# Optimization experiments

Measured on AMD Instinct MI355X. Metric: run time of the kernel, lower is better.

The kernel has to match this reference:

```python
import jax, jax.numpy as jnp
import numpy as np

B, T = 4, 512
IN, OUT, D, HID = 80, 4096, 512, 1024
E, NB, LPB = 4, 2, 4
NL = NB * LPB
H, M = 8, 64
LB, LA, SL, SR = 4, 1, 2, 1


def setup_inputs():
    key = jax.random.key(0)
    it = iter(jax.random.split(key, 40))
    def nrm(shape, s=0.02):
        return jax.random.normal(next(it), shape, jnp.float32) * s
    return {
        'x': jax.random.normal(next(it), (B, T, IN), jnp.float32),
        'seq_len': jax.random.randint(next(it), (B,), T // 2, T + 1),
        'emb_w1': nrm((IN, HID)), 'emb_b1': jnp.zeros((HID,), jnp.float32),
        'emb_w2': nrm((HID, D)), 'emb_wo': nrm((D, OUT)),
        'f0_w1': nrm((E, IN, HID)), 'f0_b1': jnp.zeros((E, HID), jnp.float32),
        'f0_w2': nrm((E, HID, D)), 'f0_router': nrm((D, E)),
        'f0_fb': nrm((LB, D), 0.1), 'f0_fa': nrm((LA, D), 0.1),
        'f_w1': nrm((NL - 1, E, D, HID)), 'f_b1': jnp.zeros((NL - 1, E, HID), jnp.float32),
        'f_w2': nrm((NL - 1, E, HID, D)), 'f_router': nrm((NL - 1, D, E)),
        'f_fb': nrm((NL - 1, LB, D), 0.1), 'f_fa': nrm((NL - 1, LA, D), 0.1),
        'attn_wq': nrm((NB, D, D)), 'attn_wk': nrm((NB, D, D)),
        'attn_wv': nrm((NB, D, D)), 'attn_wo': nrm((NB, D, D)),
        'attn_mk': nrm((NB, M, D)), 'attn_mv': nrm((NB, M, D)),
        'ln_g': jnp.ones((NB, D), jnp.float32), 'ln_b': jnp.zeros((NB, D), jnp.float32),
        'out_w': nrm((D, OUT)), 'out_b': jnp.zeros((OUT,), jnp.float32),
    }


def _fsmn_memory(p, fb, fa):
    # m[t] = p[t] + sum_k fb[k]*p[t-(k+1)*SL] + sum_j fa[j]*p[t+(j+1)*SR]  (depthwise)
    m = p
    for k in range(fb.shape[0]):
        off = (k + 1) * SL
        past = jnp.pad(p, ((0, 0), (off, 0), (0, 0)))[:, :p.shape[1]]
        m = m + past * fb[k]
    for j in range(fa.shape[0]):
        off = (j + 1) * SR
        fut = jnp.pad(p, ((0, 0), (0, off), (0, 0)))[:, off:]
        m = m + fut * fa[j]
    return m


def _pe(dtype):
    pos = jnp.arange(T, dtype=jnp.float32)[:, None]
    div = jnp.exp(jnp.arange(0, D, 2, dtype=jnp.float32) * (-np.log(10000.0) / D))
    pe = jnp.zeros((T, D), jnp.float32)
    pe = pe.at[:, 0::2].set(jnp.sin(pos * div)).at[:, 1::2].set(jnp.cos(pos * div))
    return pe.astype(dtype)


def _layernorm(x, g, b):
    mu = jnp.mean(x, -1, keepdims=True)
    var = jnp.var(x, -1, keepdims=True)
    return (x - mu) * jax.lax.rsqrt(var + 1e-5) * g + b


def reference(x, seq_len, emb_w1, emb_b1, emb_w2, emb_wo,
              f0_w1, f0_b1, f0_w2, f0_router, f0_fb, f0_fa,
              f_w1, f_b1, f_w2, f_router, f_fb, f_fa,
              attn_wq, attn_wk, attn_wv, attn_wo, attn_mk, attn_mv,
              ln_g, ln_b, out_w, out_b):
    tok_mask = jnp.arange(T)[None, :] < seq_len[:, None]  # [B,T] valid frames

    # embed sub-network (router features; detached as in Net.forward)
    embed = jax.nn.relu(x @ emb_w1 + emb_b1) @ emb_w2      # [B,T,D]
    embed_out = embed @ emb_wo                             # [B,T,OUT]
    embed_r = jax.lax.stop_gradient(embed)

    def moe_fsmn(xi, w1, b1, w2, router, fb, fa, skip):
        gates = jax.nn.softmax(embed_r @ router, axis=-1)  # [B,T,E]
        g = jnp.max(gates, axis=-1)
        disp = jax.nn.one_hot(jnp.argmax(gates, -1), E, dtype=xi.dtype) * g[..., None]
        h = jax.nn.relu(jnp.einsum('bti,eih->beth', xi, w1) + b1[None, :, None, :])
        p = jnp.einsum('beth,ehd->betd', h, w2)            # low-rank expert proj
        p = jnp.einsum('bte,betd->btd', disp, p)           # top-1 combine
        m = _fsmn_memory(p, fb, fa)
        if skip:
            m = m + xi
        imp = jnp.sum(gates * tok_mask[..., None].astype(gates.dtype), axis=(0, 1))
        aux = jnp.var(imp) / (jnp.mean(imp) ** 2 + 1e-9)   # importance cv^2
        return m, aux

    def attention(xi, wq, wk, wv, wo, mk, mv, g, b):
        dh = D // H
        q = (xi @ wq).reshape(B, T, H, dh)
        k = jnp.concatenate([xi @ wk, jnp.broadcast_to(mk, (B, M, D))], 1).reshape(B, T + M, H, dh)
        v = jnp.concatenate([xi @ wv, jnp.broadcast_to(mv, (B, M, D))], 1).reshape(B, T + M, H, dh)
        scores = jnp.einsum('bthd,bshd->bhts', q, k) / np.sqrt(dh).astype(np.float32)
        key_ok = jnp.concatenate([tok_mask, jnp.ones((B, M), bool)], 1)  # memory keys never masked
        scores = jnp.where(key_ok[:, None, None, :], scores, jnp.float32(-1e9))
        a = jax.nn.softmax(scores, -1)
        o = jnp.einsum('bhts,bshd->bthd', a, v).reshape(B, T, D) @ wo
        return _layernorm(xi + o, g, b)

    auxes = []
    cur = x
    li = 0
    for blk in range(NB):
        for _ in range(LPB):
            if li == 0:
                cur, aux = moe_fsmn(cur, f0_w1, f0_b1, f0_w2, f0_router, f0_fb, f0_fa, False)
            else:
                j = li - 1
                cur, aux = moe_fsmn(cur, f_w1[j], f_b1[j], f_w2[j], f_router[j], f_fb[j], f_fa[j], True)
            auxes.append(aux)
            li += 1
        if blk == 0:
            cur = cur + _pe(cur.dtype)[None]
        cur = attention(cur, attn_wq[blk], attn_wk[blk], attn_wv[blk], attn_wo[blk],
                        attn_mk[blk], attn_mv[blk], ln_g[blk], ln_b[blk])
    out = cur @ out_w + out_b
    return out, embed_out, jnp.stack(auxes).sum()
```

## Files before the change

kernel.cpp:

```cpp
#include <hip/hip_runtime.h>
#include <hip/hip_bf16.h>


typedef __bf16 bf16x8 __attribute__((ext_vector_type(8)));
typedef float f32x4 __attribute__((ext_vector_type(4)));

#define B_ 4
#define T_ 512
#define IN_ 80
#define OUT_ 4096
#define D_ 512
#define HID_ 1024
#define E_ 4
#define H_ 8
#define DH_ 64
#define M_ 64
#define BT_ (B_ * T_)
#define TKV_ (T_ + M_)
#define RBLK_ (BT_ / 4)

__device__ __forceinline__ unsigned pk2(float a, float b) {
    unsigned short ua = __builtin_bit_cast(unsigned short, (__bf16)a);
    unsigned short ub = __builtin_bit_cast(unsigned short, (__bf16)b);
    return (unsigned)ua | ((unsigned)ub << 16);
}
__device__ __forceinline__ unsigned pkh2(__bf16 a, __bf16 b) {
    unsigned short ua = __builtin_bit_cast(unsigned short, a);
    unsigned short ub = __builtin_bit_cast(unsigned short, b);
    return (unsigned)ua | ((unsigned)ub << 16);
}

__global__ __launch_bounds__(256) void gemm80_k(
    const float* __restrict__ A,
    const float* __restrict__ Bw,
    const float* __restrict__ bias,
    float* __restrict__ C)
{
    __shared__ float As[80][68];
    __shared__ float Bs[80][68];
    int m0 = blockIdx.y * 64, n0 = blockIdx.x * 64;
    int tid = threadIdx.x;
#pragma unroll
    for (int i = 0; i < 5; i++) {
        int idx = tid + 256 * i;
        int m = idx / 20, c = idx % 20;
        float4 f = *(const float4*)&A[(size_t)(m0 + m) * 80 + c * 4];
        As[c * 4 + 0][m] = f.x; As[c * 4 + 1][m] = f.y;
        As[c * 4 + 2][m] = f.z; As[c * 4 + 3][m] = f.w;
    }
#pragma unroll
    for (int i = 0; i < 5; i++) {
        int idx = tid + 256 * i;
        int k = idx / 16, c = idx % 16;
        float4 f = *(const float4*)&Bw[(size_t)k * 1024 + n0 + c * 4];
        *(float4*)&Bs[k][c * 4] = f;
    }
    __syncthreads();
    int tx = tid & 15, ty = tid >> 4;
    float acc[4][4];
#pragma unroll
    for (int j = 0; j < 4; j++)
#pragma unroll
        for (int i = 0; i < 4; i++) acc[j][i] = 0.f;
#pragma unroll 8
    for (int k = 0; k < 80; k++) {
        float4 a = *(const float4*)&As[k][ty * 4];
        float4 b = *(const float4*)&Bs[k][tx * 4];
        float av[4] = {a.x, a.y, a.z, a.w};
        float bv[4] = {b.x, b.y, b.z, b.w};
#pragma unroll
        for (int j = 0; j < 4; j++)
#pragma unroll
            for (int i = 0; i < 4; i++) acc[j][i] += av[j] * bv[i];
    }
#pragma unroll
    for (int j = 0; j < 4; j++) {
        size_t row = (size_t)(m0 + ty * 4 + j);
        float4 o;
        o.x = fmaxf(acc[j][0] + bias[n0 + tx * 4 + 0], 0.f);
        o.y = fmaxf(acc[j][1] + bias[n0 + tx * 4 + 1], 0.f);
        o.z = fmaxf(acc[j][2] + bias[n0 + tx * 4 + 2], 0.f);
        o.w = fmaxf(acc[j][3] + bias[n0 + tx * 4 + 3], 0.f);
        *(float4*)&C[row * 1024 + n0 + tx * 4] = o;
    }
}

__global__ void wr2_k(const float* __restrict__ w2,
                      const float* __restrict__ r0,
                      const float* __restrict__ rl,
                      float* __restrict__ R2)
{
    int wv = threadIdx.x >> 6, lane = threadIdx.x & 63;
    int h = blockIdx.x * 4 + wv;
    const float* wrow = w2 + (size_t)h * 512;
    float w[8];
#pragma unroll
    for (int i = 0; i < 8; i++) w[i] = wrow[lane + 64 * i];
    for (int l = 0; l < 8; l++) {
        const float* rp = (l == 0) ? r0 : rl + (size_t)(l - 1) * 2048;
        double a0 = 0, a1 = 0, a2 = 0, a3 = 0;
#pragma unroll
        for (int i = 0; i < 8; i++) {
            int d = lane + 64 * i;
            float4 r = *(const float4*)&rp[d * 4];
            a0 += (double)w[i] * (double)r.x;
            a1 += (double)w[i] * (double)r.y;
            a2 += (double)w[i] * (double)r.z;
            a3 += (double)w[i] * (double)r.w;
        }
        for (int off = 32; off; off >>= 1) {
            a0 += __shfl_xor(a0, off); a1 += __shfl_xor(a1, off);
            a2 += __shfl_xor(a2, off); a3 += __shfl_xor(a3, off);
        }
        if (lane == 0) {
            float4 o = make_float4((float)a0, (float)a1, (float)a2, (float)a3);
            *(float4*)&R2[((size_t)l * 1024 + h) * 4] = o;
        }
    }
}

__global__ __launch_bounds__(256) void routerall_k(
    const float* __restrict__ h,
    const float* __restrict__ R2,
    const int* __restrict__ seq_len,
    int* __restrict__ eid,
    float* __restrict__ gatev,
    float* __restrict__ impPart)
{
    __shared__ float impLoc[4][32];
    int wv = threadIdx.x >> 6, lane = threadIdx.x & 63;
    int tok = blockIdx.x * 4 + wv;
    const float* hr = h + (size_t)tok * 1024;
    float acc[8][4];
#pragma unroll
    for (int l = 0; l < 8; l++)
#pragma unroll
        for (int e = 0; e < 4; e++) acc[l][e] = 0.f;
    for (int i = 0; i < 16; i++) {
        int d = lane + 64 * i;
        float hv = hr[d];
#pragma unroll
        for (int l = 0; l < 8; l++) {
            float4 r = *(const float4*)&R2[((size_t)l * 1024 + d) * 4];
            acc[l][0] += hv * r.x; acc[l][1] += hv * r.y;
            acc[l][2] += hv * r.z; acc[l][3] += hv * r.w;
        }
    }
    for (int off = 32; off; off >>= 1) {
#pragma unroll
        for (int l = 0; l < 8; l++)
#pragma unroll
            for (int e = 0; e < 4; e++) acc[l][e] += __shfl_xor(acc[l][e], off);
    }
    if (lane == 0) {
        int b = tok >> 9, t = tok & 511;
        bool valid = t < seq_len[b];
        for (int l = 0; l < 8; l++) {
            float lg[4] = {acc[l][0], acc[l][1], acc[l][2], acc[l][3]};
            float mx = fmaxf(fmaxf(lg[0], lg[1]), fmaxf(lg[2], lg[3]));
            float g[4], s = 0.f;
            for (int e = 0; e < 4; e++) { g[e] = expf(lg[e] - mx); s += g[e]; }
            float inv = 1.f / s;
            int am = 0; float bv = g[0];
            for (int e = 1; e < 4; e++) if (g[e] > bv) { bv = g[e]; am = e; }
            eid[l * BT_ + tok] = am;
            gatev[l * BT_ + tok] = bv * inv;
            for (int e = 0; e < 4; e++)
                impLoc[wv][l * 4 + e] = valid ? g[e] * inv : 0.f;
        }
    }
    __syncthreads();
    int tid = threadIdx.x;
    if (tid < 32) {
        float s = impLoc[0][tid] + impLoc[1][tid] + impLoc[2][tid] + impLoc[3][tid];
        impPart[(size_t)blockIdx.x * 32 + tid] = s;
    }
}

__global__ void cvtw_k(const float* __restrict__ src, __bf16* __restrict__ dst,
                       int nsh, int kpsh, int Ksrc)
{
    int idx = blockIdx.x * 256 + threadIdx.x;
    int cprsh = nsh - 3;
    int row = idx >> cprsh;
    int chunk = idx & ((1 << cprsh) - 1);
    int e = row >> kpsh, k = row & ((1 << kpsh) - 1);
    int n = chunk * 8;
    uint4 pk;
    if (k < Ksrc) {
        const float* sp = src + (((size_t)e * Ksrc + k) << nsh) + n;
        float4 f0 = *(const float4*)sp;
        float4 f1 = *(const float4*)(sp + 4);
        pk = make_uint4(pk2(f0.x, f0.y), pk2(f0.z, f0.w),
                        pk2(f1.x, f1.y), pk2(f1.z, f1.w));
    } else pk = make_uint4(0, 0, 0, 0);
    *(uint4*)&dst[(((size_t)row) << nsh) + n] = pk;
}

__global__ void gathera_k(const float* __restrict__ src, int lda,
                          const int* __restrict__ sorted,
                          __bf16* __restrict__ dst, int kpsh, int Ksrc)
{
    int idx = blockIdx.x * 256 + threadIdx.x;
    int cprsh = kpsh - 3;
    int row = idx >> cprsh;
    int chunk = idx & ((1 << cprsh) - 1);
    int k0 = chunk * 8;
    uint4 pk;
    if (k0 < Ksrc) {
        const float* sp = src + (size_t)sorted[row] * lda + k0;
        float4 f0 = *(const float4*)sp;
        float4 f1 = *(const float4*)(sp + 4);
        pk = make_uint4(pk2(f0.x, f0.y), pk2(f0.z, f0.w),
                        pk2(f1.x, f1.y), pk2(f1.z, f1.w));
    } else pk = make_uint4(0, 0, 0, 0);
    *(uint4*)&dst[((size_t)row << kpsh) + k0] = pk;
}

template<bool W1OUT>
__global__ __launch_bounds__(256) void egemm_k(
    const __bf16* __restrict__ Ag, const __bf16* __restrict__ Bh,
    const float* __restrict__ bias,
    __bf16* __restrict__ Cb, float* __restrict__ Cf,
    int N, int Kpad,
    const int* __restrict__ seg, const int* __restrict__ sorted,
    const float* __restrict__ scale)
{
    __shared__ __align__(16) __bf16 As[2][128 * 64];
    __shared__ __align__(16) __bf16 Bs[2][64 * 64];

    int e = blockIdx.z;
    int row0 = seg[e], cnt = seg[e + 1] - row0;
    int m0 = blockIdx.y * 128;
    if (m0 >= cnt) return;
    int n0 = blockIdx.x * 64;
    const __bf16* Bp = Bh + (size_t)e * Kpad * N;

    int tid = threadIdx.x;
    int arow = tid >> 1, ahalf = tid & 1;
    const __bf16* aptr = Ag + (size_t)(row0 + m0 + arow) * Kpad + ahalf * 32;
    int asb = arow * 64;
    int ac0 = ahalf * 4;
    int arx = arow & 7;
    int bn = tid & 63, bkc = tid >> 6;
    const __bf16* bptr = Bp + n0 + bn;
    int bsb = bn * 64;
    int brx = bn & 7;

    int lane = tid & 63, wid = tid >> 6;
    int wm = wid & 1, wn = wid >> 1;
    int l15 = lane & 15, quad = lane >> 4;

    int aoff[4][2], boff[2][2];
#pragma unroll
    for (int mt = 0; mt < 4; mt++) {
        int m = wm * 64 + mt * 16 + l15;
#pragma unroll
        for (int s = 0; s < 2; s++)
            aoff[mt][s] = m * 64 + (((s * 4 + quad) ^ (m & 7)) * 8);
    }
#pragma unroll
    for (int nt = 0; nt < 2; nt++) {
        int n = wn * 32 + nt * 16 + l15;
#pragma unroll
        for (int s = 0; s < 2; s++)
            boff[nt][s] = n * 64 + (((s * 4 + quad) ^ (n & 7)) * 8);
    }

    f32x4 acc[4][2];
#pragma unroll
    for (int mt = 0; mt < 4; mt++)
#pragma unroll
        for (int nt = 0; nt < 2; nt++)
#pragma unroll
            for (int r = 0; r < 4; r++) acc[mt][nt][r] = 0.f;

    uint4 rA[4]; unsigned rB[8];
    auto stage = [&](int k0) {
#pragma unroll
        for (int j = 0; j < 4; j++) rA[j] = *(const uint4*)(aptr + k0 + j * 8);
#pragma unroll
        for (int c = 0; c < 2; c++) {
            int kk = k0 + (bkc * 2 + c) * 8;
#pragma unroll
            for (int i = 0; i < 4; i++)
                rB[c * 4 + i] = pkh2(bptr[(size_t)(kk + 2 * i) * N],
                                     bptr[(size_t)(kk + 2 * i + 1) * N]);
        }
    };
    auto commit = [&](int buf) {
#pragma unroll
        for (int j = 0; j < 4; j++)
            *(uint4*)&As[buf][asb + (((ac0 + j) ^ arx) * 8)] = rA[j];
#pragma unroll
        for (int c = 0; c < 2; c++)
            *(uint4*)&Bs[buf][bsb + (((bkc * 2 + c) ^ brx) * 8)] =
                make_uint4(rB[c * 4 + 0], rB[c * 4 + 1], rB[c * 4 + 2], rB[c * 4 + 3]);
    };

    stage(0); commit(0); __syncthreads();
    int nt_ = Kpad >> 6;
    for (int t = 0; t < nt_; t++) {
        int buf = t & 1;
        if (t + 1 < nt_) stage((t + 1) << 6);
        bf16x8 af[4][2], bfr[2][2];
#pragma unroll
        for (int mt = 0; mt < 4; mt++)
#pragma unroll
            for (int s = 0; s < 2; s++)
                af[mt][s] = *(const bf16x8*)&As[buf][aoff[mt][s]];
#pragma unroll
        for (int ntx = 0; ntx < 2; ntx++)
#pragma unroll
            for (int s = 0; s < 2; s++)
                bfr[ntx][s] = *(const bf16x8*)&Bs[buf][boff[ntx][s]];
#pragma unroll
        for (int mt = 0; mt < 4; mt++)
#pragma unroll
            for (int ntx = 0; ntx < 2; ntx++)
#pragma unroll
                for (int s = 0; s < 2; s++)
                    acc[mt][ntx] = __builtin_amdgcn_mfma_f32_16x16x32_bf16(
                        af[mt][s], bfr[ntx][s], acc[mt][ntx], 0, 0, 0);
        if (t + 1 < nt_) commit(buf ^ 1);
        __syncthreads();
    }

#pragma unroll
    for (int mt = 0; mt < 4; mt++) {
#pragma unroll
        for (int r = 0; r < 4; r++) {
            int m = m0 + wm * 64 + mt * 16 + quad * 4 + r;
            if (m >= cnt) continue;
            if (W1OUT) {
                size_t ci = (size_t)(row0 + m);
#pragma unroll
                for (int ntx = 0; ntx < 2; ntx++) {
                    int col = n0 + wn * 32 + ntx * 16 + l15;
                    float v = acc[mt][ntx][r] + bias[e * N + col];
                    Cb[ci * N + col] = (__bf16)fmaxf(v, 0.f);
                }
            } else {
                int tok = sorted[row0 + m];
                float sc = scale[tok];
#pragma unroll
                for (int ntx = 0; ntx < 2; ntx++) {
                    int col = n0 + wn * 32 + ntx * 16 + l15;
                    Cf[(size_t)tok * N + col] = acc[mt][ntx][r] * sc;
                }
            }
        }
    }
}

template<bool BIAS>
__global__ __launch_bounds__(256) void dgemm_k(
    const float* __restrict__ A,
    const __bf16* __restrict__ Bh,
    const float* __restrict__ bias,
    float* __restrict__ C,
    int N, int K)
{
    __shared__ __align__(16) __bf16 As[2][128 * 64];
    __shared__ __align__(16) __bf16 Bs[2][64 * 64];

    int m0 = blockIdx.y * 128, n0 = blockIdx.x * 64;
    int tid = threadIdx.x;
    int arow = tid >> 1, ahalf = tid & 1;
    const float* aptr = A + (size_t)(m0 + arow) * K + ahalf * 32;
    int asb = arow * 64, ac0 = ahalf * 4, arx = arow & 7;
    int bn = tid & 63, bkc = tid >> 6;
    const __bf16* bptr = Bh + n0 + bn;
    int bsb = bn * 64, brx = bn & 7;

    int lane = tid & 63, wid = tid >> 6;
    int wm = wid & 1, wn = wid >> 1;
    int l15 = lane & 15, quad = lane >> 4;

    int aoff[4][2], boff[2][2];
#pragma unroll
    for (int mt = 0; mt < 4; mt++) {
        int m = wm * 64 + mt * 16 + l15;
#pragma unroll
        for (int s = 0; s < 2; s++)
            aoff[mt][s] = m * 64 + (((s * 4 + quad) ^ (m & 7)) * 8);
    }
#pragma unroll
    for (int nt = 0; nt < 2; nt++) {
        int n = wn * 32 + nt * 16 + l15;
#pragma unroll
        for (int s = 0; s < 2; s++)
            boff[nt][s] = n * 64 + (((s * 4 + quad) ^ (n & 7)) * 8);
    }

    f32x4 acc[4][2];
#pragma unroll
    for (int mt = 0; mt < 4; mt++)
#pragma unroll
        for (int nt = 0; nt < 2; nt++)
#pragma unroll
            for (int r = 0; r < 4; r++) acc[mt][nt][r] = 0.f;

    uint4 rA[4]; unsigned rB[8];
    auto stage = [&](int k0) {
#pragma unroll
        for (int j = 0; j < 4; j++) {
            float4 f0 = *(const float4*)(aptr + k0 + j * 8);
            float4 f1 = *(const float4*)(aptr + k0 + j * 8 + 4);
            rA[j] = make_uint4(pk2(f0.x, f0.y), pk2(f0.z, f0.w),
                               pk2(f1.x, f1.y), pk2(f1.z, f1.w));
        }
#pragma unroll
        for (int c = 0; c < 2; c++) {
            int kk = k0 + (bkc * 2 + c) * 8;
#pragma unroll
            for (int i = 0; i < 4; i++)
                rB[c * 4 + i] = pkh2(bptr[(size_t)(kk + 2 * i) * N],
                                     bptr[(size_t)(kk + 2 * i + 1) * N]);
        }
    };
    auto commit = [&](int buf) {
#pragma unroll
        for (int j = 0; j < 4; j++)
            *(uint4*)&As[buf][asb + (((ac0 + j) ^ arx) * 8)] = rA[j];
#pragma unroll
        for (int c = 0; c < 2; c++)
            *(uint4*)&Bs[buf][bsb + (((bkc * 2 + c) ^ brx) * 8)] =
                make_uint4(rB[c * 4 + 0], rB[c * 4 + 1], rB[c * 4 + 2], rB[c * 4 + 3]);
    };

    stage(0); commit(0); __syncthreads();
    int nt_ = K >> 6;
    for (int t = 0; t < nt_; t++) {
        int buf = t & 1;
        if (t + 1 < nt_) stage((t + 1) << 6);
        bf16x8 af[4][2], bfr[2][2];
#pragma unroll
        for (int mt = 0; mt < 4; mt++)
#pragma unroll
            for (int s = 0; s < 2; s++)
                af[mt][s] = *(const bf16x8*)&As[buf][aoff[mt][s]];
#pragma unroll
        for (int ntx = 0; ntx < 2; ntx++)
#pragma unroll
            for (int s = 0; s < 2; s++)
                bfr[ntx][s] = *(const bf16x8*)&Bs[buf][boff[ntx][s]];
#pragma unroll
        for (int mt = 0; mt < 4; mt++)
#pragma unroll
            for (int ntx = 0; ntx < 2; ntx++)
#pragma unroll
                for (int s = 0; s < 2; s++)
                    acc[mt][ntx] = __builtin_amdgcn_mfma_f32_16x16x32_bf16(
                        af[mt][s], bfr[ntx][s], acc[mt][ntx], 0, 0, 0);
        if (t + 1 < nt_) commit(buf ^ 1);
        __syncthreads();
    }

#pragma unroll
    for (int mt = 0; mt < 4; mt++) {
#pragma unroll
        for (int r = 0; r < 4; r++) {
            int m = m0 + wm * 64 + mt * 16 + quad * 4 + r;
#pragma unroll
            for (int ntx = 0; ntx < 2; ntx++) {
                int col = n0 + wn * 32 + ntx * 16 + l15;
                float v = acc[mt][ntx][r];
                if (BIAS) v += bias[col];
                C[(size_t)m * N + col] = v;
            }
        }
    }
}

#define MBM 128
#define MBN 64
#define MBK 32
#define LDAS 40

__global__ __launch_bounds__(256) void qkv_k(
    const float* __restrict__ A,
    const __bf16* __restrict__ wq, const __bf16* __restrict__ wk,
    const __bf16* __restrict__ wv,
    float* __restrict__ qo, float* __restrict__ ko, float* __restrict__ vo)
{
    __shared__ __align__(16) __bf16 As[MBM * LDAS];
    __shared__ __align__(16) __bf16 Bs[MBN * LDAS];

    int n0g = blockIdx.x * MBN;
    int which = n0g >> 9;
    int n0 = n0g & 511;
    const __bf16* Bp = (which == 0) ? wq : (which == 1) ? wk : wv;
    float* Cp = (which == 0) ? qo : (which == 1) ? ko : vo;
    int m0 = blockIdx.y * MBM;

    int tid = threadIdx.x;
    int arow = tid >> 1, ahalf = tid & 1;
    const float* aptr = A + (size_t)(m0 + arow) * D_ + ahalf * 16;
    int asw = (arow >> 3) & 3;
    int bn = tid & 63, bkc = tid >> 6;
    int bcs = bkc ^ ((bn >> 3) & 3);

    int lane = tid & 63, wid = tid >> 6;
    int wm = wid & 1, wn = wid >> 1;
    int l15 = lane & 15, quad = lane >> 4;

    int aoff[4], boff[2];
#pragma unroll
    for (int mt = 0; mt < 4; mt++) {
        int m = wm * 64 + mt * 16 + l15;
        aoff[mt] = m * LDAS + (quad ^ ((m >> 3) & 3)) * 8;
    }
#pragma unroll
    for (int nt = 0; nt < 2; nt++) {
        int n = wn * 32 + nt * 16 + l15;
        boff[nt] = n * LDAS + (quad ^ ((n >> 3) & 3)) * 8;
    }

    f32x4 acc[4][2];
#pragma unroll
    for (int mt = 0; mt < 4; mt++)
#pragma unroll
        for (int nt = 0; nt < 2; nt++)
#pragma unroll
            for (int r = 0; r < 4; r++) acc[mt][nt][r] = 0.f;

    for (int k0 = 0; k0 < D_; k0 += MBK) {
#pragma unroll
        for (int cc = 0; cc < 2; cc++) {
            float4 f0 = *(const float4*)(aptr + k0 + cc * 8);
            float4 f1 = *(const float4*)(aptr + k0 + cc * 8 + 4);
            uint4 pk = make_uint4(pk2(f0.x, f0.y), pk2(f0.z, f0.w),
                                  pk2(f1.x, f1.y), pk2(f1.z, f1.w));
            int cs = (ahalf * 2 + cc) ^ asw;
            *(uint4*)&As[arow * LDAS + cs * 8] = pk;
        }
        {
            __bf16 f[8];
            int kk = k0 + bkc * 8;
#pragma unroll
            for (int i = 0; i < 8; i++)
                f[i] = Bp[(size_t)(kk + i) * D_ + n0 + bn];
            uint4 pk = make_uint4(pkh2(f[0], f[1]), pkh2(f[2], f[3]),
                                  pkh2(f[4], f[5]), pkh2(f[6], f[7]));
            *(uint4*)&Bs[bn * LDAS + bcs * 8] = pk;
        }
        __syncthreads();
        bf16x8 af[4], bfm[2];
#pragma unroll
        for (int mt = 0; mt < 4; mt++) af[mt] = *(const bf16x8*)&As[aoff[mt]];
#pragma unroll
        for (int nt = 0; nt < 2; nt++) bfm[nt] = *(const bf16x8*)&Bs[boff[nt]];
#pragma unroll
        for (int mt = 0; mt < 4; mt++)
#pragma unroll
            for (int nt = 0; nt < 2; nt++)
                acc[mt][nt] = __builtin_amdgcn_mfma_f32_16x16x32_bf16(
                    af[mt], bfm[nt], acc[mt][nt], 0, 0, 0);
        __syncthreads();
    }

#pragma unroll
    for (int mt = 0; mt < 4; mt++) {
#pragma unroll
        for (int r = 0; r < 4; r++) {
            int mi = wm * 64 + mt * 16 + quad * 4 + r;
            int m = m0 + mi;
            size_t crow = which ? (size_t)(m + (m >> 9) * M_) : (size_t)m;
#pragma unroll
            for (int nt = 0; nt < 2; nt++) {
                int col = n0 + wn * 32 + nt * 16 + l15;
                Cp[crow * (size_t)D_ + col] = acc[mt][nt][r];
            }
        }
    }
}

__global__ void bucketall_k(const int* __restrict__ eidA, int* __restrict__ sortedA,
                            int* __restrict__ segA)
{
    __shared__ int cnt[E_]; __shared__ int cur[E_];
    int l = blockIdx.x;
    const int* eid = eidA + l * BT_;
    int* sorted = sortedA + l * BT_;
    int* seg = segA + l * 8;
    int tid = threadIdx.x;
    if (tid < E_) cnt[tid] = 0;
    __syncthreads();
    for (int t = tid; t < BT_; t += 256) atomicAdd(&cnt[eid[t]], 1);
    __syncthreads();
    if (tid == 0) {
        int o = 0;
        for (int e = 0; e < E_; e++) { seg[e] = o; cur[e] = o; o += cnt[e]; }
        seg[E_] = o;
    }
    __syncthreads();
    for (int t = tid; t < BT_; t += 256) {
        int pos = atomicAdd(&cur[eid[t]], 1);
        sorted[pos] = t;
    }
}

__global__ void fsmn_k(const float* __restrict__ p, const float* __restrict__ fb,
                       const float* __restrict__ fa, float* __restrict__ cur, int skip)
{
    int idx = blockIdx.x * 256 + threadIdx.x;
    int d = idx & 511;
    int t = (idx >> 9) & 511;
    float m = p[idx];
#pragma unroll
    for (int k = 0; k < 4; k++) {
        int tt = t - 2 * (k + 1);
        if (tt >= 0) m += fb[k * D_ + d] * p[idx - D_ * 2 * (k + 1)];
    }
    if (t + 1 < T_) m += fa[d] * p[idx + D_];
    if (skip) m += cur[idx];
    cur[idx] = m;
}

__global__ void addpe_k(float* __restrict__ cur) {
    int idx = blockIdx.x * 256 + threadIdx.x;
    int d = idx & 511, t = (idx >> 9) & 511;
    float div = expf((float)(d & ~1) * (-9.210340371976184f / (float)D_));
    float ang = (float)t * div;
    cur[idx] += (d & 1) ? cosf(ang) : sinf(ang);
}

__global__ void fillmem_k(const float* __restrict__ mk, const float* __restrict__ mv,
                          float* __restrict__ kbuf, float* __restrict__ vbuf)
{
    int idx = blockIdx.x * 256 + threadIdx.x;
    int d = idx & 511, m = (idx >> 9) & 63, b = idx >> 15;
    size_t row = (size_t)b * TKV_ + T_ + m;
    kbuf[row * D_ + d] = mk[m * D_ + d];
    vbuf[row * D_ + d] = mv[m * D_ + d];
}

#define QR 16
__global__ __launch_bounds__(256) void attn_k(
    const float* __restrict__ q, const float* __restrict__ kbuf,
    const float* __restrict__ vbuf, const int* __restrict__ seq_len,
    float* __restrict__ attno)
{
    __shared__ float kv[64 * 68];
    __shared__ float qs[QR][68];
    __shared__ float sc[QR][584];
    int b = blockIdx.z, h = blockIdx.y, t0 = blockIdx.x * QR;
    int tid = threadIdx.x, w = tid >> 6, lane = tid & 63;
    int r0 = w * 4;
#pragma unroll
    for (int i = 0; i < 4; i++) {
        int idx = tid + 256 * i;
        int r = idx >> 6, d = idx & 63;
        qs[r][d] = q[((size_t)(b * T_) + t0 + r) * D_ + h * DH_ + d] * 0.125f;
    }
    int sl = seq_len[b];
    int ntv = (sl + 63) >> 6;
    int kg = lane & 15, quad = lane >> 4;
    int myrow = r0 + quad;

    for (int ti = 0; ti <= ntv; ti++) {
        int t = (ti < ntv) ? ti : 8;
        int s0 = t * 64;
        __syncthreads();
        {
            const float* kp = kbuf + ((size_t)b * TKV_ + s0 + w * 16) * D_ + h * DH_ + lane;
#pragma unroll
            for (int jj = 0; jj < 4; jj++) {
                float4 kf;
                kf.x = kp[(jj * 4 + 0) * D_];
                kf.y = kp[(jj * 4 + 1) * D_];
                kf.z = kp[(jj * 4 + 2) * D_];
                kf.w = kp[(jj * 4 + 3) * D_];
                *(float4*)&kv[lane * 68 + w * 16 + jj * 4] = kf;
            }
        }
        __syncthreads();
        float a0 = 0, a1 = 0, a2 = 0, a3 = 0;
#pragma unroll 8
        for (int d = 0; d < 64; d++) {
            float4 kf = *(const float4*)&kv[d * 68 + kg * 4];
            float qv = qs[myrow][d];
            a0 = fmaf(qv, kf.x, a0);
            a1 = fmaf(qv, kf.y, a1);
            a2 = fmaf(qv, kf.z, a2);
            a3 = fmaf(qv, kf.w, a3);
        }
        int sb = s0 + kg * 4;
        float4 o;
        o.x = (sb + 0 >= T_ || sb + 0 < sl) ? a0 : -1e9f;
        o.y = (sb + 1 >= T_ || sb + 1 < sl) ? a1 : -1e9f;
        o.z = (sb + 2 >= T_ || sb + 2 < sl) ? a2 : -1e9f;
        o.w = (sb + 3 >= T_ || sb + 3 < sl) ? a3 : -1e9f;
        *(float4*)&sc[myrow][s0 + kg * 4] = o;
    }
    __syncthreads();

    float inv[4];
#pragma unroll
    for (int r = 0; r < 4; r++) {
        float mx = -1e30f;
        for (int ti = 0; ti <= ntv; ti++) {
            int s0 = ((ti < ntv) ? ti : 8) * 64;
            mx = fmaxf(mx, sc[r0 + r][s0 + lane]);
        }
        for (int off = 32; off; off >>= 1) mx = fmaxf(mx, __shfl_xor(mx, off));
        float sum = 0.f;
        for (int ti = 0; ti <= ntv; ti++) {
            int s0 = ((ti < ntv) ? ti : 8) * 64;
            float e2 = expf(sc[r0 + r][s0 + lane] - mx);
            sc[r0 + r][s0 + lane] = e2; sum += e2;
        }
        for (int off = 32; off; off >>= 1) sum += __shfl_xor(sum, off);
        inv[r] = 1.f / sum;
    }

    float o0 = 0, o1 = 0, o2 = 0, o3 = 0;
    for (int ti = 0; ti <= ntv; ti++) {
        int t = (ti < ntv) ? ti : 8;
        int s0 = t * 64;
        __syncthreads();
#pragma unroll
        for (int i = 0; i < 16; i++) {
            int idx = tid + 256 * i;
            int key = idx >> 6, d = idx & 63;
            kv[key * 68 + d] = vbuf[((size_t)b * TKV_ + s0 + key) * D_ + h * DH_ + d];
        }
        __syncthreads();
#pragma unroll 4
        for (int g = 0; g < 16; g++) {
            float4 p0 = *(const float4*)&sc[r0 + 0][s0 + g * 4];
            float4 p1 = *(const float4*)&sc[r0 + 1][s0 + g * 4];
            float4 p2 = *(const float4*)&sc[r0 + 2][s0 + g * 4];
            float4 p3 = *(const float4*)&sc[r0 + 3][s0 + g * 4];
            float v0 = kv[(g * 4 + 0) * 68 + lane];
            float v1 = kv[(g * 4 + 1) * 68 + lane];
            float v2 = kv[(g * 4 + 2) * 68 + lane];
            float v3 = kv[(g * 4 + 3) * 68 + lane];
            o0 += p0.x * v0 + p0.y * v1 + p0.z * v2 + p0.w * v3;
            o1 += p1.x * v0 + p1.y * v1 + p1.z * v2 + p1.w * v3;
            o2 += p2.x * v0 + p2.y * v1 + p2.z * v2 + p2.w * v3;
            o3 += p3.x * v0 + p3.y * v1 + p3.z * v2 + p3.w * v3;
        }
    }
    size_t base = ((size_t)(b * T_) + t0 + r0) * D_ + h * DH_ + lane;
    attno[base + 0 * D_] = o0 * inv[0];
    attno[base + 1 * D_] = o1 * inv[1];
    attno[base + 2 * D_] = o2 * inv[2];
    attno[base + 3 * D_] = o3 * inv[3];
}

__global__ void ln_k(const float* __restrict__ o, const float* __restrict__ g,
                     const float* __restrict__ bb, float* __restrict__ cur)
{
    int w = threadIdx.x >> 6, lane = threadIdx.x & 63;
    size_t row = (size_t)(blockIdx.x * 4 + w);
    float v[8]; float s = 0.f;
#pragma unroll
    for (int i = 0; i < 8; i++) {
        int d = lane + 64 * i;
        v[i] = cur[row * D_ + d] + o[row * D_ + d];
        s += v[i];
    }
    for (int off = 32; off; off >>= 1) s += __shfl_xor(s, off);
    float mu = s * (1.f / D_);
    float vs = 0.f;
#pragma unroll
    for (int i = 0; i < 8; i++) { float dd = v[i] - mu; vs += dd * dd; }
    for (int off = 32; off; off >>= 1) vs += __shfl_xor(vs, off);
    float rstd = rsqrtf(vs * (1.f / D_) + 1e-5f);
#pragma unroll
    for (int i = 0; i < 8; i++) {
        int d = lane + 64 * i;
        cur[row * D_ + d] = (v[i] - mu) * rstd * g[d] + bb[d];
    }
}

__global__ __launch_bounds__(256) void aux_k(const float* __restrict__ impPart,
                                             float* __restrict__ outp)
{
    __shared__ float red[8][32];
    __shared__ float imp[32];
    int tid = threadIdx.x;
    int c = tid & 31, p = tid >> 5;
    float s = 0.f;
    for (int b = p; b < RBLK_; b += 8) s += impPart[(size_t)b * 32 + c];
    red[p][c] = s;
    __syncthreads();
    if (tid < 32) {
        float t = 0.f;
#pragma unroll
        for (int i = 0; i < 8; i++) t += red[i][tid];
        imp[tid] = t;
    }
    __syncthreads();
    if (tid == 0) {
        float total = 0.f;
        for (int l = 0; l < 8; l++) {
            const float* ip = imp + l * 4;
            float m = (ip[0] + ip[1] + ip[2] + ip[3]) * 0.25f;
            float var = 0.f;
            for (int e = 0; e < 4; e++) { float d = ip[e] - m; var += d * d; }
            var *= 0.25f;
            total += var / (m * m + 1e-9f);
        }
        *outp = total;
    }
}

extern "C" void kernel_launch(void* const* d_in, const int* in_sizes, int n_in,
                              void* d_out, int out_size, void* d_ws, size_t ws_size,
                              hipStream_t stream)
{
    (void)in_sizes; (void)n_in; (void)out_size; (void)ws_size;
    const float* x        = (const float*)d_in[0];
    const int*   seqlen   = (const int*)d_in[1];
    const float* emb_w1   = (const float*)d_in[2];
    const float* emb_b1   = (const float*)d_in[3];
    const float* emb_w2   = (const float*)d_in[4];
    const float* emb_wo   = (const float*)d_in[5];
    const float* f0_w1    = (const float*)d_in[6];
    const float* f0_b1    = (const float*)d_in[7];
    const float* f0_w2    = (const float*)d_in[8];
    const float* f0_router= (const float*)d_in[9];
    const float* f0_fb    = (const float*)d_in[10];
    const float* f0_fa    = (const float*)d_in[11];
    const float* f_w1     = (const float*)d_in[12];
    const float* f_b1     = (const float*)d_in[13];
    const float* f_w2     = (const float*)d_in[14];
    const float* f_router = (const float*)d_in[15];
    const float* f_fb     = (const float*)d_in[16];
    const float* f_fa     = (const float*)d_in[17];
    const float* attn_wq  = (const float*)d_in[18];
    const float* attn_wk  = (const float*)d_in[19];
    const float* attn_wv  = (const float*)d_in[20];
    const float* attn_wo  = (const float*)d_in[21];
    const float* attn_mk  = (const float*)d_in[22];
    const float* attn_mv  = (const float*)d_in[23];
    const float* ln_g     = (const float*)d_in[24];
    const float* ln_b     = (const float*)d_in[25];
    const float* out_w    = (const float*)d_in[26];
    const float* out_b    = (const float*)d_in[27];

    float* out0 = (float*)d_out;
    float* out1 = out0 + (size_t)BT_ * OUT_;
    float* out2 = out1 + (size_t)BT_ * OUT_;

    float* fws = (float*)d_ws;
    size_t o = 0;
    float* embedF = fws + o; o += (size_t)BT_ * D_;
    float* curB   = fws + o; o += (size_t)BT_ * D_;
    float* hbuf   = fws + o; o += (size_t)BT_ * HID_;
    float* pbuf   = fws + o; o += (size_t)BT_ * D_;
    float* kbuf   = fws + o; o += (size_t)B_ * TKV_ * D_;
    float* vbuf   = fws + o; o += (size_t)B_ * TKV_ * D_;
    float* gatev  = fws + o; o += (size_t)8 * BT_;
    float* impPart= fws + o; o += (size_t)RBLK_ * 32;
    float* R2     = fws + o; o += (size_t)8 * 1024 * 4;
    int* eid     = (int*)(fws + o); o += (size_t)8 * BT_;
    int* sortedA = (int*)(fws + o); o += (size_t)8 * BT_;
    int* segA    = (int*)(fws + o); o += 64;
    __bf16* Ag    = (__bf16*)hbuf;
    __bf16* hbufh = (__bf16*)(hbuf + (size_t)BT_ * D_ / 2);
    __bf16* w1h   = (__bf16*)kbuf;
    __bf16* w2h   = (__bf16*)vbuf;
    __bf16* w2e_h = (__bf16*)vbuf;
    __bf16* woe_h = (__bf16*)kbuf;
    __bf16* outw_h= (__bf16*)kbuf;
    __bf16* wqh   = (__bf16*)embedF;
    __bf16* wkh   = wqh + (size_t)D_ * D_;
    __bf16* wvh   = wkh + (size_t)D_ * D_;
    __bf16* woh   = wvh + (size_t)D_ * D_;
    float* qbuf  = pbuf;
    float* attno = hbuf;
    float* tmpo  = hbuf + (size_t)BT_ * D_;

    gemm80_k<<<dim3(HID_ / 64, BT_ / 64, 1), 256, 0, stream>>>(x, emb_w1, emb_b1, hbuf);
    wr2_k<<<256, 256, 0, stream>>>(emb_w2, f0_router, f_router, R2);
    routerall_k<<<RBLK_, 256, 0, stream>>>(hbuf, R2, seqlen, eid, gatev, impPart);
    bucketall_k<<<8, 256, 0, stream>>>(eid, sortedA, segA);
    cvtw_k<<<256, 256, 0, stream>>>(emb_w2, w2e_h, 9, 10, HID_);
    cvtw_k<<<1024, 256, 0, stream>>>(emb_wo, woe_h, 12, 9, D_);
    dgemm_k<false><<<dim3(D_ / 64, BT_ / 128, 1), 256, 0, stream>>>(
        hbuf, w2e_h, nullptr, embedF, D_, HID_);
    dgemm_k<false><<<dim3(OUT_ / 64, BT_ / 128, 1), 256, 0, stream>>>(
        embedF, woe_h, nullptr, out1, OUT_, D_);

    for (int l = 0; l < 8; l++) {
        const float* w1  = (l == 0) ? f0_w1 : f_w1 + (size_t)(l-1) * E_ * D_ * HID_;
        const float* b1p = (l == 0) ? f0_b1 : f_b1 + (size_t)(l-1) * E_ * HID_;
        const float* w2  = (l == 0) ? f0_w2 : f_w2 + (size_t)(l-1) * E_ * HID_ * D_;
        const float* fbp = (l == 0) ? f0_fb : f_fb + (size_t)(l-1) * 4 * D_;
        const float* fap = (l == 0) ? f0_fa : f_fa + (size_t)(l-1) * 1 * D_;
        const float* Ain = (l == 0) ? x : curB;
        int lda  = (l == 0) ? IN_ : D_;
        int Ks   = (l == 0) ? IN_ : D_;
        int Kp   = (l == 0) ? 128 : 512;
        int kpsh = (l == 0) ? 7 : 9;
        const int* seg = segA + l * 8;
        const int* sorted = sortedA + l * BT_;

        cvtw_k<<<E_ * Kp * HID_ / 8 / 256, 256, 0, stream>>>(w1, w1h, 10, kpsh, Ks);
        cvtw_k<<<E_ * HID_ * D_ / 8 / 256, 256, 0, stream>>>(w2, w2h, 9, 10, HID_);
        gathera_k<<<BT_ * Kp / 8 / 256, 256, 0, stream>>>(Ain, lda, sorted, Ag, kpsh, Ks);

        egemm_k<true><<<dim3(HID_/64, BT_/128, E_), 256, 0, stream>>>(
            Ag, w1h, b1p, hbufh, nullptr, HID_, Kp, seg, nullptr, nullptr);
        egemm_k<false><<<dim3(D_/64, BT_/128, E_), 256, 0, stream>>>(
            hbufh, w2h, nullptr, nullptr, pbuf, D_, HID_, seg, sorted, gatev + l * BT_);
        fsmn_k<<<BT_*D_/256, 256, 0, stream>>>(pbuf, fbp, fap, curB, (l > 0) ? 1 : 0);

        if (l == 3) addpe_k<<<BT_*D_/256, 256, 0, stream>>>(curB);

        if (l == 3 || l == 7) {
            int ab = (l == 3) ? 0 : 1;
            const float* wq = attn_wq + (size_t)ab * D_ * D_;
            const float* wk = attn_wk + (size_t)ab * D_ * D_;
            const float* wv = attn_wv + (size_t)ab * D_ * D_;
            const float* wo = attn_wo + (size_t)ab * D_ * D_;
            const float* mk = attn_mk + (size_t)ab * M_ * D_;
            const float* mv = attn_mv + (size_t)ab * M_ * D_;
            const float* g  = ln_g + (size_t)ab * D_;
            const float* bb = ln_b + (size_t)ab * D_;

            cvtw_k<<<128, 256, 0, stream>>>(wq, wqh, 9, 9, D_);
            cvtw_k<<<128, 256, 0, stream>>>(wk, wkh, 9, 9, D_);
            cvtw_k<<<128, 256, 0, stream>>>(wv, wvh, 9, 9, D_);
            cvtw_k<<<128, 256, 0, stream>>>(wo, woh, 9, 9, D_);
            qkv_k<<<dim3(3 * D_ / MBN, BT_ / MBM, 1), 256, 0, stream>>>(
                curB, wqh, wkh, wvh, qbuf, kbuf, vbuf);
            fillmem_k<<<B_*M_*D_/256, 256, 0, stream>>>(mk, mv, kbuf, vbuf);
            attn_k<<<dim3(T_/QR, H_, B_), 256, 0, stream>>>(qbuf, kbuf, vbuf, seqlen, attno);
            dgemm_k<false><<<dim3(D_ / 64, BT_ / 128, 1), 256, 0, stream>>>(
                attno, woh, nullptr, tmpo, D_, D_);
            ln_k<<<BT_/4, 256, 0, stream>>>(tmpo, g, bb, curB);
        }
    }

    cvtw_k<<<1024, 256, 0, stream>>>(out_w, outw_h, 12, 9, D_);
    dgemm_k<true><<<dim3(OUT_ / 64, BT_ / 128, 1), 256, 0, stream>>>(
        curB, outw_h, out_b, out0, OUT_, D_);
    aux_k<<<1, 256, 0, stream>>>(impPart, out2);
}
```

Measured before the change: 1.424 ms.

## Merge prep kernels, fuse PE into FSMN, read fp32 attention weights and memory directly

The three per-layer weight-conversion and gather launches become a single prep_k launch. Positional encoding is folded into fsmn_k. The attention weight bf16 conversions are dropped: qkv_k and dgemm_k now read fp32 weights and convert on the fly. fillmem_k is removed because attn_k reads the memory keys and values straight from mk/mv. An A-row clamp is also added in egemm_k. Together these cut launch count and intermediate traffic, at the cost of redundant fp32 weight loads and conversion inside the GEMM tiles.

```diff
diff --git a/kernel.cpp b/kernel.cpp
--- a/kernel.cpp
+++ b/kernel.cpp
@@ -177,10 +177,10 @@
     }
 }
 
-__global__ void cvtw_k(const float* __restrict__ src, __bf16* __restrict__ dst,
-                       int nsh, int kpsh, int Ksrc)
-{
-    int idx = blockIdx.x * 256 + threadIdx.x;
+__device__ __forceinline__ void cvt_body(const float* __restrict__ src,
+                                         __bf16* __restrict__ dst,
+                                         int idx, int nsh, int kpsh, int Ksrc)
+{
     int cprsh = nsh - 3;
     int row = idx >> cprsh;
     int chunk = idx & ((1 << cprsh) - 1);
@@ -197,11 +197,11 @@
     *(uint4*)&dst[(((size_t)row) << nsh) + n] = pk;
 }
 
-__global__ void gathera_k(const float* __restrict__ src, int lda,
-                          const int* __restrict__ sorted,
-                          __bf16* __restrict__ dst, int kpsh, int Ksrc)
-{
-    int idx = blockIdx.x * 256 + threadIdx.x;
+__device__ __forceinline__ void gather_body(const float* __restrict__ src, int lda,
+                                            const int* __restrict__ sorted,
+                                            __bf16* __restrict__ dst,
+                                            int idx, int kpsh, int Ksrc)
+{
     int cprsh = kpsh - 3;
     int row = idx >> cprsh;
     int chunk = idx & ((1 << cprsh) - 1);
@@ -217,6 +217,30 @@
     *(uint4*)&dst[((size_t)row << kpsh) + k0] = pk;
 }
 
+__global__ void cvtw_k(const float* __restrict__ src, __bf16* __restrict__ dst,
+                       int nsh, int kpsh, int Ksrc)
+{
+    cvt_body(src, dst, blockIdx.x * 256 + threadIdx.x, nsh, kpsh, Ksrc);
+}
+
+__global__ void prep_k(const float* __restrict__ w1, const float* __restrict__ w2,
+                       const float* __restrict__ Ain, int lda,
+                       const int* __restrict__ sorted,
+                       __bf16* __restrict__ w1h, __bf16* __restrict__ w2h,
+                       __bf16* __restrict__ Ag,
+                       int kpsh, int Ks, int nb1, int nb2)
+{
+    int bx = blockIdx.x;
+    if (bx < nb1) {
+        cvt_body(w1, w1h, bx * 256 + threadIdx.x, 10, kpsh, Ks);
+    } else if (bx < nb1 + nb2) {
+        cvt_body(w2, w2h, (bx - nb1) * 256 + threadIdx.x, 9, 10, HID_);
+    } else {
+        gather_body(Ain, lda, sorted, Ag, (bx - nb1 - nb2) * 256 + threadIdx.x,
+                    kpsh, Ks);
+    }
+}
+
 template<bool W1OUT>
 __global__ __launch_bounds__(256) void egemm_k(
     const __bf16* __restrict__ Ag, const __bf16* __restrict__ Bh,
@@ -238,7 +262,8 @@
 
     int tid = threadIdx.x;
     int arow = tid >> 1, ahalf = tid & 1;
-    const __bf16* aptr = Ag + (size_t)(row0 + m0 + arow) * Kpad + ahalf * 32;
+    int mclamp = min(m0 + arow, cnt - 1);
+    const __bf16* aptr = Ag + (size_t)(row0 + mclamp) * Kpad + ahalf * 32;
     int asb = arow * 64;
     int ac0 = ahalf * 4;
     int arx = arow & 7;
@@ -353,10 +378,10 @@
     }
 }
 
-template<bool BIAS>
+template<bool BIAS, bool BF16B>
 __global__ __launch_bounds__(256) void dgemm_k(
     const float* __restrict__ A,
-    const __bf16* __restrict__ Bh,
+    const void* __restrict__ Bv,
     const float* __restrict__ bias,
     float* __restrict__ C,
     int N, int K)
@@ -370,7 +395,8 @@
     const float* aptr = A + (size_t)(m0 + arow) * K + ahalf * 32;
     int asb = arow * 64, ac0 = ahalf * 4, arx = arow & 7;
     int bn = tid & 63, bkc = tid >> 6;
-    const __bf16* bptr = Bh + n0 + bn;
+    const __bf16* bh = (const __bf16*)Bv;
+    const float*  bf = (const float*)Bv;
     int bsb = bn * 64, brx = bn & 7;
 
     int lane = tid & 63, wid = tid >> 6;
@@ -414,9 +440,14 @@
         for (int c = 0; c < 2; c++) {
             int kk = k0 + (bkc * 2 + c) * 8;
 #pragma unroll
-            for (int i = 0; i < 4; i++)
-                rB[c * 4 + i] = pkh2(bptr[(size_t)(kk + 2 * i) * N],
-                                     bptr[(size_t)(kk + 2 * i + 1) * N]);
+            for (int i = 0; i < 4; i++) {
+                if (BF16B)
+                    rB[c * 4 + i] = pkh2(bh[(size_t)(kk + 2 * i) * N + n0 + bn],
+                                         bh[(size_t)(kk + 2 * i + 1) * N + n0 + bn]);
+                else
+                    rB[c * 4 + i] = pk2(bf[(size_t)(kk + 2 * i) * N + n0 + bn],
+                                        bf[(size_t)(kk + 2 * i + 1) * N + n0 + bn]);
+            }
         }
     };
     auto commit = [&](int buf) {
@@ -480,8 +511,8 @@
 
 __global__ __launch_bounds__(256) void qkv_k(
     const float* __restrict__ A,
-    const __bf16* __restrict__ wq, const __bf16* __restrict__ wk,
-    const __bf16* __restrict__ wv,
+    const float* __restrict__ wq, const float* __restrict__ wk,
+    const float* __restrict__ wv,
     float* __restrict__ qo, float* __restrict__ ko, float* __restrict__ vo)
 {
     __shared__ __align__(16) __bf16 As[MBM * LDAS];
@@ -490,7 +521,7 @@
     int n0g = blockIdx.x * MBN;
     int which = n0g >> 9;
     int n0 = n0g & 511;
-    const __bf16* Bp = (which == 0) ? wq : (which == 1) ? wk : wv;
+    const float* Bp = (which == 0) ? wq : (which == 1) ? wk : wv;
     float* Cp = (which == 0) ? qo : (which == 1) ? ko : vo;
     int m0 = blockIdx.y * MBM;
 
@@ -536,13 +567,13 @@
             *(uint4*)&As[arow * LDAS + cs * 8] = pk;
         }
         {
-            __bf16 f[8];
+            float f[8];
             int kk = k0 + bkc * 8;
 #pragma unroll
             for (int i = 0; i < 8; i++)
                 f[i] = Bp[(size_t)(kk + i) * D_ + n0 + bn];
-            uint4 pk = make_uint4(pkh2(f[0], f[1]), pkh2(f[2], f[3]),
-                                  pkh2(f[4], f[5]), pkh2(f[6], f[7]));
+            uint4 pk = make_uint4(pk2(f[0], f[1]), pk2(f[2], f[3]),
+                                  pk2(f[4], f[5]), pk2(f[6], f[7]));
             *(uint4*)&Bs[bn * LDAS + bcs * 8] = pk;
         }
         __syncthreads();
@@ -566,11 +597,10 @@
         for (int r = 0; r < 4; r++) {
             int mi = wm * 64 + mt * 16 + quad * 4 + r;
             int m = m0 + mi;
-            size_t crow = which ? (size_t)(m + (m >> 9) * M_) : (size_t)m;
 #pragma unroll
             for (int nt = 0; nt < 2; nt++) {
                 int col = n0 + wn * 32 + nt * 16 + l15;
-                Cp[crow * (size_t)D_ + col] = acc[mt][nt][r];
+                Cp[(size_t)m * D_ + col] = acc[mt][nt][r];
             }
         }
     }
@@ -602,7 +632,8 @@
 }
 
 __global__ void fsmn_k(const float* __restrict__ p, const float* __restrict__ fb,
-                       const float* __restrict__ fa, float* __restrict__ cur, int skip)
+                       const float* __restrict__ fa, float* __restrict__ cur,
+                       int skip, int pe)
 {
     int idx = blockIdx.x * 256 + threadIdx.x;
     int d = idx & 511;
@@ -615,31 +646,19 @@
     }
     if (t + 1 < T_) m += fa[d] * p[idx + D_];
     if (skip) m += cur[idx];
+    if (pe) {
+        float div = expf((float)(d & ~1) * (-9.210340371976184f / (float)D_));
+        float ang = (float)t * div;
+        m += (d & 1) ? cosf(ang) : sinf(ang);
+    }
     cur[idx] = m;
-}
-
-__global__ void addpe_k(float* __restrict__ cur) {
-    int idx = blockIdx.x * 256 + threadIdx.x;
-    int d = idx & 511, t = (idx >> 9) & 511;
-    float div = expf((float)(d & ~1) * (-9.210340371976184f / (float)D_));
-    float ang = (float)t * div;
-    cur[idx] += (d & 1) ? cosf(ang) : sinf(ang);
-}
-
-__global__ void fillmem_k(const float* __restrict__ mk, const float* __restrict__ mv,
-                          float* __restrict__ kbuf, float* __restrict__ vbuf)
-{
-    int idx = blockIdx.x * 256 + threadIdx.x;
-    int d = idx & 511, m = (idx >> 9) & 63, b = idx >> 15;
-    size_t row = (size_t)b * TKV_ + T_ + m;
-    kbuf[row * D_ + d] = mk[m * D_ + d];
-    vbuf[row * D_ + d] = mv[m * D_ + d];
 }
 
 #define QR 16
 __global__ __launch_bounds__(256) void attn_k(
     const float* __restrict__ q, const float* __restrict__ kbuf,
-    const float* __restrict__ vbuf, const int* __restrict__ seq_len,
+    const float* __restrict__ vbuf, const float* __restrict__ mk,
+    const float* __restrict__ mv, const int* __restrict__ seq_len,
     float* __restrict__ attno)
 {
     __shared__ float kv[64 * 68];
@@ -664,7 +683,9 @@
         int s0 = t * 64;
         __syncthreads();
         {
-            const float* kp = kbuf + ((size_t)b * TKV_ + s0 + w * 16) * D_ + h * DH_ + lane;
+            const float* kp = (t < 8)
+                ? kbuf + ((size_t)(b * T_) + s0 + w * 16) * D_ + h * DH_ + lane
+                : mk + (size_t)(w * 16) * D_ + h * DH_ + lane;
 #pragma unroll
             for (int jj = 0; jj < 4; jj++) {
                 float4 kf;
@@ -724,7 +745,10 @@
         for (int i = 0; i < 16; i++) {
             int idx = tid + 256 * i;
             int key = idx >> 6, d = idx & 63;
-            kv[key * 68 + d] = vbuf[((size_t)b * TKV_ + s0 + key) * D_ + h * DH_ + d];
+            const float* vp = (t < 8)
+                ? vbuf + ((size_t)(b * T_) + s0 + key) * D_ + h * DH_ + d
+                : mv + (size_t)key * D_ + h * DH_ + d;
+            kv[key * 68 + d] = *vp;
         }
         __syncthreads();
 #pragma unroll 4
@@ -852,8 +876,8 @@
     float* curB   = fws + o; o += (size_t)BT_ * D_;
     float* hbuf   = fws + o; o += (size_t)BT_ * HID_;
     float* pbuf   = fws + o; o += (size_t)BT_ * D_;
-    float* kbuf   = fws + o; o += (size_t)B_ * TKV_ * D_;
-    float* vbuf   = fws + o; o += (size_t)B_ * TKV_ * D_;
+    float* kbuf   = fws + o; o += (size_t)BT_ * D_;
+    float* vbuf   = fws + o; o += (size_t)BT_ * D_;
     float* gatev  = fws + o; o += (size_t)8 * BT_;
     float* impPart= fws + o; o += (size_t)RBLK_ * 32;
     float* R2     = fws + o; o += (size_t)8 * 1024 * 4;
@@ -867,10 +891,6 @@
     __bf16* w2e_h = (__bf16*)vbuf;
     __bf16* woe_h = (__bf16*)kbuf;
     __bf16* outw_h= (__bf16*)kbuf;
-    __bf16* wqh   = (__bf16*)embedF;
-    __bf16* wkh   = wqh + (size_t)D_ * D_;
-    __bf16* wvh   = wkh + (size_t)D_ * D_;
-    __bf16* woh   = wvh + (size_t)D_ * D_;
     float* qbuf  = pbuf;
     float* attno = hbuf;
     float* tmpo  = hbuf + (size_t)BT_ * D_;
@@ -881,9 +901,9 @@
     bucketall_k<<<8, 256, 0, stream>>>(eid, sortedA, segA);
     cvtw_k<<<256, 256, 0, stream>>>(emb_w2, w2e_h, 9, 10, HID_);
     cvtw_k<<<1024, 256, 0, stream>>>(emb_wo, woe_h, 12, 9, D_);
-    dgemm_k<false><<<dim3(D_ / 64, BT_ / 128, 1), 256, 0, stream>>>(
+    dgemm_k<false,true><<<dim3(D_ / 64, BT_ / 128, 1), 256, 0, stream>>>(
         hbuf, w2e_h, nullptr, embedF, D_, HID_);
-    dgemm_k<false><<<dim3(OUT_ / 64, BT_ / 128, 1), 256, 0, stream>>>(
+    dgemm_k<false,true><<<dim3(OUT_ / 64, BT_ / 128, 1), 256, 0, stream>>>(
         embedF, woe_h, nullptr, out1, OUT_, D_);
 
     for (int l = 0; l < 8; l++) {
@@ -900,17 +920,19 @@
         const int* seg = segA + l * 8;
         const int* sorted = sortedA + l * BT_;
 
-        cvtw_k<<<E_ * Kp * HID_ / 8 / 256, 256, 0, stream>>>(w1, w1h, 10, kpsh, Ks);
-        cvtw_k<<<E_ * HID_ * D_ / 8 / 256, 256, 0, stream>>>(w2, w2h, 9, 10, HID_);
-        gathera_k<<<BT_ * Kp / 8 / 256, 256, 0, stream>>>(Ain, lda, sorted, Ag, kpsh, Ks);
+        int nb1 = E_ * Kp * HID_ / 8 / 256;
+        int nb2 = E_ * HID_ * D_ / 8 / 256;
+        int nb3 = BT_ * Kp / 8 / 256;
+        prep_k<<<nb1 + nb2 + nb3, 256, 0, stream>>>(
+            w1, w2, Ain, lda, sorted, w1h, w2h, Ag, kpsh, Ks, nb1, nb2);
 
         egemm_k<true><<<dim3(HID_/64, BT_/128, E_), 256, 0, stream>>>(
             Ag, w1h, b1p, hbufh, nullptr, HID_, Kp, seg, nullptr, nullptr);
         egemm_k<false><<<dim3(D_/64, BT_/128, E_), 256, 0, stream>>>(
-            hbufh, w2h, nullptr, nullptr, pbuf, D_, HID_, seg, sorted, gatev + l * BT_);
-        fsmn_k<<<BT_*D_/256, 256, 0, stream>>>(pbuf, fbp, fap, curB, (l > 0) ? 1 : 0);
-
-        if (l == 3) addpe_k<<<BT_*D_/256, 256, 0, stream>>>(curB);
+            hbufh, w2h, nullptr, nullptr, pbuf, D_, HID_, seg, sorted,
+            gatev + l * BT_);
+        fsmn_k<<<BT_*D_/256, 256, 0, stream>>>(pbuf, fbp, fap, curB,
+                                               (l > 0) ? 1 : 0, (l == 3) ? 1 : 0);
 
         if (l == 3 || l == 7) {
             int ab = (l == 3) ? 0 : 1;
@@ -923,22 +945,18 @@
             const float* g  = ln_g + (size_t)ab * D_;
             const float* bb = ln_b + (size_t)ab * D_;
 
-            cvtw_k<<<128, 256, 0, stream>>>(wq, wqh, 9, 9, D_);
-            cvtw_k<<<128, 256, 0, stream>>>(wk, wkh, 9, 9, D_);
-            cvtw_k<<<128, 256, 0, stream>>>(wv, wvh, 9, 9, D_);
-            cvtw_k<<<128, 256, 0, stream>>>(wo, woh, 9, 9, D_);
             qkv_k<<<dim3(3 * D_ / MBN, BT_ / MBM, 1), 256, 0, stream>>>(
-                curB, wqh, wkh, wvh, qbuf, kbuf, vbuf);
-            fillmem_k<<<B_*M_*D_/256, 256, 0, stream>>>(mk, mv, kbuf, vbuf);
-            attn_k<<<dim3(T_/QR, H_, B_), 256, 0, stream>>>(qbuf, kbuf, vbuf, seqlen, attno);
-            dgemm_k<false><<<dim3(D_ / 64, BT_ / 128, 1), 256, 0, stream>>>(
-                attno, woh, nullptr, tmpo, D_, D_);
+                curB, wq, wk, wv, qbuf, kbuf, vbuf);
+            attn_k<<<dim3(T_/QR, H_, B_), 256, 0, stream>>>(
+                qbuf, kbuf, vbuf, mk, mv, seqlen, attno);
+            dgemm_k<false,false><<<dim3(D_ / 64, BT_ / 128, 1), 256, 0, stream>>>(
+                attno, wo, nullptr, tmpo, D_, D_);
             ln_k<<<BT_/4, 256, 0, stream>>>(tmpo, g, bb, curB);
         }
     }
 
     cvtw_k<<<1024, 256, 0, stream>>>(out_w, outw_h, 12, 9, D_);
-    dgemm_k<true><<<dim3(OUT_ / 64, BT_ / 128, 1), 256, 0, stream>>>(
+    dgemm_k<true,true><<<dim3(OUT_ / 64, BT_ / 128, 1), 256, 0, stream>>>(
         curB, outw_h, out_b, out0, OUT_, D_);
     aux_k<<<1, 256, 0, stream>>>(impPart, out2);
 }
```

After: 1.384 ms. -2.8%, faster.
